# Kernel optimization log

Measured on AMD Instinct MI355X. Metric: run time of the kernel, lower is better.

The kernel has to match this reference:

```python
import jax, jax.numpy as jnp
import numpy as np

SEQ_LEN, PRED_LEN, PATCH_LEN, STRIDE, NUM_LAYERS = 512, 96, 16, 4, 2
NUM_QUBITS = 4
NUM_PATCHES = (SEQ_LEN - PATCH_LEN) // STRIDE + 1  # 125


def setup_inputs() -> dict:
    key = jax.random.key(0)
    k1, k2, k3, k4 = jax.random.split(key, 4)
    x = jax.random.normal(k1, (64, SEQ_LEN, 64), dtype=jnp.float32)
    weights = jax.random.uniform(k2, (NUM_LAYERS, NUM_QUBITS, 3), dtype=jnp.float32) * (2 * np.pi)
    head_w = jax.random.normal(k3, (PRED_LEN, NUM_PATCHES * NUM_QUBITS), dtype=jnp.float32) * 0.04
    head_b = jax.random.normal(k4, (PRED_LEN,), dtype=jnp.float32) * 0.01
    return {"x": x, "weights": weights, "head_w": head_w, "head_b": head_b}


def _apply_rot(state, phi, theta, omega, wire):
    # Rot = RZ(omega) RY(theta) RZ(phi); PennyLane wire 0 is MSB -> tensor axis wire+1
    c = jnp.cos(0.5 * theta)
    s = jnp.sin(0.5 * theta)
    e = lambda a: jnp.exp(1j * a)
    half, diff = 0.5 * (phi + omega), 0.5 * (phi - omega)
    U = jnp.stack([jnp.stack([e(-half) * c, -e(diff) * s]),
                   jnp.stack([e(-diff) * s, e(half) * c])]).astype(jnp.complex64)  # [2,2]
    st = jnp.moveaxis(state, wire + 1, -1)
    st = st @ U.T  # new_j = sum_k U[j,k] old_k
    return jnp.moveaxis(st, -1, wire + 1)


def _cnot(state, c, t):
    # flip target axis where control bit == 1
    mshape = [1, 1, 1, 1, 1]
    mshape[c + 1] = 2
    mask = (jnp.arange(2) == 1).reshape(mshape)
    return jnp.where(mask, jnp.flip(state, axis=t + 1), state)


def _quantum_encoder(patches, weights):
    # patches: [N,16] real; AmplitudeEmbedding(normalize=True)
    psi = patches / jnp.linalg.norm(patches, axis=-1, keepdims=True)
    state = psi.astype(jnp.complex64).reshape(-1, 2, 2, 2, 2)  # [N,2,2,2,2], wire0=MSB
    for l in range(NUM_LAYERS):
        for q in range(NUM_QUBITS):
            state = _apply_rot(state, weights[l, q, 0], weights[l, q, 1], weights[l, q, 2], q)
        r = (l % (NUM_QUBITS - 1)) + 1  # default StronglyEntanglingLayers ranges
        for i in range(NUM_QUBITS):
            state = _cnot(state, i, (i + r) % NUM_QUBITS)
    probs = jnp.abs(state.reshape(-1, 16)) ** 2  # [N,16]
    # <Z_q> = sum_k p_k * (1 - 2*bit_q(k)), wire0 = MSB of 4-bit index
    bits = (np.arange(16)[:, None] >> (NUM_QUBITS - 1 - np.arange(NUM_QUBITS))[None, :]) & 1
    signs = jnp.asarray(1.0 - 2.0 * bits, dtype=jnp.float32)  # [16,4]
    return probs @ signs  # [N,4]


def reference(x, weights, head_w, head_b):
    B, L, M = x.shape
    xs = jnp.transpose(x, (0, 2, 1)).reshape(B * M, L)
    idx = np.arange(NUM_PATCHES)[:, None] * STRIDE + np.arange(PATCH_LEN)[None, :]
    xp = xs[:, idx].reshape(-1, PATCH_LEN) + 1e-6  # [B*M*NP, 16]
    enc = _quantum_encoder(xp, weights)  # [B*M*NP, 4]
    enc = enc.reshape(B * M, NUM_PATCHES * NUM_QUBITS)
    out = enc @ head_w.T + head_b  # [B*M, pred_len]
    return jnp.transpose(out.reshape(B, M, PRED_LEN), (0, 2, 1))
```

## Files before the change

### kernel.cpp

```cpp
#include <hip/hip_runtime.h>
#include <cmath>

#define BATCH 64
#define SEQLEN 512
#define NFEAT 64
#define NPATCH 125
#define PREDLEN 96
#define NCOLS 500

#define MG 8
#define XROW 528
#define ELD 520

typedef __attribute__((ext_vector_type(8))) short short8;
typedef __attribute__((ext_vector_type(4))) short short4v;
typedef __attribute__((ext_vector_type(4))) float f32x4;

__device__ __forceinline__ unsigned short f2bf(float f) {
    unsigned int u = __float_as_uint(f);
    u += 0x7FFFu + ((u >> 16) & 1u);
    return (unsigned short)(u >> 16);
}
__device__ __forceinline__ float bf2f(unsigned short h) {
    return __uint_as_float(((unsigned int)h) << 16);
}
__device__ __forceinline__ unsigned int cvtpk(float a, float b) {
    unsigned int r;
    asm volatile("v_cvt_pk_bf16_f32 %0, %1, %2" : "=v"(r) : "v"(a), "v"(b));
    return r;
}

__global__ __launch_bounds__(512) void qml_one(
    const float* __restrict__ x,
    const float* __restrict__ w,
    const float* __restrict__ hw,
    const float* __restrict__ hb,
    float* __restrict__ out)
{
    __shared__ float G[32 * 16];
    __shared__ unsigned short xh[MG][XROW];
    __shared__ unsigned short xl[MG][XROW];
    __shared__ unsigned short enc[MG][ELD];

    const int tid  = threadIdx.x;
    const int lane = tid & 63;
    const int lr   = lane & 15;
    const int kg   = lane >> 4;
    const int wv   = tid >> 6;

    const int idx = blockIdx.x;
    const int b   = ((idx >> 6) << 3) | (idx & 7);
    const int m0  = ((idx >> 3) & 7) * MG;

    if (wv == 0) {
        float my[8];
        {
            const int  g      = lane & 7;
            const float phi   = w[g * 3 + 0];
            const float theta = w[g * 3 + 1];
            const float omega = w[g * 3 + 2];
            const float c  = cosf(0.5f * theta), s  = sinf(0.5f * theta);
            const float hf = 0.5f * (phi + omega), df = 0.5f * (phi - omega);
            const float ch = cosf(hf), sh = sinf(hf);
            const float cd = cosf(df), sd = sinf(df);
            my[0] =  ch * c;  my[1] = -sh * c;
            my[2] = -cd * s;  my[3] = -sd * s;
            my[4] =  cd * s;  my[5] = -sd * s;
            my[6] =  ch * c;  my[7] =  sh * c;
        }
        float re[16], im[16];
        #pragma unroll
        for (int k = 0; k < 16; ++k) { re[k] = (k == (lane & 15)) ? 1.f : 0.f; im[k] = 0.f; }
        #pragma unroll
        for (int l = 0; l < 2; ++l) {
            #pragma unroll
            for (int qq = 0; qq < 4; ++qq) {
                const int g = l * 4 + qq;
                const float u00r = __shfl(my[0], g), u00i = __shfl(my[1], g);
                const float u01r = __shfl(my[2], g), u01i = __shfl(my[3], g);
                const float u10r = __shfl(my[4], g), u10i = __shfl(my[5], g);
                const float u11r = __shfl(my[6], g), u11i = __shfl(my[7], g);
                const int bit = 8 >> qq;
                #pragma unroll
                for (int k = 0; k < 16; ++k) {
                    if (k & bit) continue;
                    const int k1 = k | bit;
                    const float a0r = re[k],  a0i = im[k];
                    const float a1r = re[k1], a1i = im[k1];
                    re[k]  = u00r * a0r - u00i * a0i + u01r * a1r - u01i * a1i;
                    im[k]  = u00r * a0i + u00i * a0r + u01r * a1i + u01i * a1r;
                    re[k1] = u10r * a0r - u10i * a0i + u11r * a1r - u11i * a1i;
                    im[k1] = u10r * a0i + u10i * a0r + u11r * a1i + u11i * a1r;
                }
            }
            const int r = (l % 3) + 1;
            #pragma unroll
            for (int i = 0; i < 4; ++i) {
                const int cb = 8 >> i;
                const int tb = 8 >> ((i + r) & 3);
                #pragma unroll
                for (int k = 0; k < 16; ++k) {
                    if ((k & cb) && !(k & tb)) {
                        const int k1 = k | tb;
                        float t;
                        t = re[k]; re[k] = re[k1]; re[k1] = t;
                        t = im[k]; im[k] = im[k1]; im[k1] = t;
                    }
                }
            }
        }
        if (lane < 16) {
            #pragma unroll
            for (int k = 0; k < 16; ++k) {
                G[k * 16 + lane]        = re[k];
                G[(16 + k) * 16 + lane] = im[k];
            }
        }
    } else {
        const float* xb = x + (size_t)b * SEQLEN * NFEAT + m0;
        unsigned int* xh32[8]; unsigned int* xl32[8];
        #pragma unroll
        for (int c = 0; c < 8; ++c) {
            xh32[c] = reinterpret_cast<unsigned int*>(&xh[c][0]);
            xl32[c] = reinterpret_cast<unsigned int*>(&xl[c][0]);
        }
        for (int u = tid - 64; u < XROW / 2; u += 448) {
            const int t = 2 * u;
            float4 a0, a1, b0, b1;
            if (t < SEQLEN) {
                const float* base = xb + (size_t)t * NFEAT;
                a0 = *reinterpret_cast<const float4*>(base);
                a1 = *reinterpret_cast<const float4*>(base + 4);
                b0 = *reinterpret_cast<const float4*>(base + NFEAT);
                b1 = *reinterpret_cast<const float4*>(base + NFEAT + 4);
            } else {
                a0 = make_float4(0.f, 0.f, 0.f, 0.f);
                a1 = a0; b0 = a0; b1 = a0;
            }
            const float av[8] = {a0.x, a0.y, a0.z, a0.w, a1.x, a1.y, a1.z, a1.w};
            const float bv[8] = {b0.x, b0.y, b0.z, b0.w, b1.x, b1.y, b1.z, b1.w};
            #pragma unroll
            for (int c = 0; c < 8; ++c) {
                const float va = av[c] + 1e-6f;
                const float vb = bv[c] + 1e-6f;
                const unsigned int h = cvtpk(va, vb);
                xh32[c][u] = h;
                const float ra = va - __uint_as_float(h << 16);
                const float rb = vb - __uint_as_float(h & 0xFFFF0000u);
                xl32[c][u] = cvtpk(ra, rb);
            }
        }
    }
    __syncthreads();

    short8 ah0, al0, ah1, al1;
    {
        const int koff = (kg & 1) * 8;
        #pragma unroll
        for (int c = 0; c < 8; ++c) {
            const float g0 = G[lr * 16 + koff + c];
            const unsigned short h0 = f2bf(g0);
            ah0[c] = (short)h0;
            al0[c] = (short)f2bf(g0 - bf2f(h0));
            const float g1 = G[(16 + lr) * 16 + koff + c];
            const unsigned short h1 = f2bf(g1);
            ah1[c] = (short)h1;
            al1[c] = (short)f2bf(g1 - bf2f(h1));
        }
    }

    {
        const int m = wv;
        const unsigned short* xrow = (kg < 2) ? &xh[m][0] : &xl[m][0];
        #pragma unroll 1
        for (int nt = 0; nt < 8; ++nt) {
            const int p = nt * 16 + lr;

            const short4v* src = reinterpret_cast<const short4v*>(xrow + 4 * p + (kg & 1) * 8);
            const short4v s0 = src[0];
            const short4v s1 = src[1];
            short8 bfrag;
            #pragma unroll
            for (int c = 0; c < 4; ++c) { bfrag[c] = s0[c]; bfrag[c + 4] = s1[c]; }

            const f32x4 zz = {0.f, 0.f, 0.f, 0.f};
            f32x4 acc0 = __builtin_amdgcn_mfma_f32_16x16x32_bf16(al0, bfrag, zz, 0, 0, 0);
            acc0 = __builtin_amdgcn_mfma_f32_16x16x32_bf16(ah0, bfrag, acc0, 0, 0, 0);
            f32x4 acc1 = __builtin_amdgcn_mfma_f32_16x16x32_bf16(al1, bfrag, zz, 0, 0, 0);
            acc1 = __builtin_amdgcn_mfma_f32_16x16x32_bf16(ah1, bfrag, acc1, 0, 0, 0);

            const float p0 = acc0[0] * acc0[0] + acc1[0] * acc1[0];
            const float p1 = acc0[1] * acc0[1] + acc1[1] * acc1[1];
            const float p2 = acc0[2] * acc0[2] + acc1[2] * acc1[2];
            const float p3 = acc0[3] * acc0[3] + acc1[3] * acc1[3];
            const float psum = (p0 + p1) + (p2 + p3);
            float s0v = (kg & 2) ? psum : 0.f;
            float s1v = (kg & 1) ? psum : 0.f;
            float s2v = p2 + p3;
            float s3v = p1 + p3;
            float sav = psum;
            s0v += __shfl_xor(s0v, 16); s0v += __shfl_xor(s0v, 32);
            s1v += __shfl_xor(s1v, 16); s1v += __shfl_xor(s1v, 32);
            s2v += __shfl_xor(s2v, 16); s2v += __shfl_xor(s2v, 32);
            s3v += __shfl_xor(s3v, 16); s3v += __shfl_xor(s3v, 32);
            sav += __shfl_xor(sav, 16); sav += __shfl_xor(sav, 32);

            const float rinv = 1.f / sav;
            const float ssel = (kg == 0) ? s0v : (kg == 1) ? s1v : (kg == 2) ? s2v : s3v;
            const float zval = 1.f - 2.f * ssel * rinv;
            enc[m][4 * p + kg] = (p < NPATCH) ? f2bf(zval) : (unsigned short)0;
        }
    }
    __syncthreads();

    if (wv < 6) {
        const int o = wv * 16 + lr;
        const float* hwrow = hw + (size_t)o * NCOLS;
        const unsigned short* erow = &enc[lr & 7][0];

        f32x4 acc = {0.f, 0.f, 0.f, 0.f};
        #pragma unroll 2
        for (int kc = 0; kc < 15; ++kc) {
            const int k0 = kc * 32 + kg * 8;
            const short8 e  = *reinterpret_cast<const short8*>(erow + k0);
            const float4 w0 = *reinterpret_cast<const float4*>(hwrow + k0);
            const float4 w1 = *reinterpret_cast<const float4*>(hwrow + k0 + 4);
            union { unsigned int u[4]; short8 s; } wf;
            wf.u[0] = cvtpk(w0.x, w0.y);
            wf.u[1] = cvtpk(w0.z, w0.w);
            wf.u[2] = cvtpk(w1.x, w1.y);
            wf.u[3] = cvtpk(w1.z, w1.w);
            acc = __builtin_amdgcn_mfma_f32_16x16x32_bf16(e, wf.s, acc, 0, 0, 0);
        }
        {
            const int k0 = 480 + kg * 8;
            const short8 e = *reinterpret_cast<const short8*>(erow + k0);
            short8 wf;
            #pragma unroll
            for (int c = 0; c < 8; ++c) {
                const int k = k0 + c;
                wf[c] = (k < NCOLS) ? (short)f2bf(hwrow[k]) : (short)0;
            }
            acc = __builtin_amdgcn_mfma_f32_16x16x32_bf16(e, wf, acc, 0, 0, 0);
        }

        if (kg < 2) {
            const float bias = hb[o];
            #pragma unroll
            for (int j = 0; j < 4; ++j) {
                const int m = m0 + 4 * kg + j;
                out[((size_t)b * PREDLEN + o) * NFEAT + m] = acc[j] + bias;
            }
        }
    }
}

extern "C" void kernel_launch(void* const* d_in, const int* in_sizes, int n_in,
                              void* d_out, int out_size, void* d_ws, size_t ws_size,
                              hipStream_t stream) {
    const float* x  = (const float*)d_in[0];
    const float* w  = (const float*)d_in[1];
    const float* hw = (const float*)d_in[2];
    const float* hb = (const float*)d_in[3];
    float* out = (float*)d_out;

    (void)d_ws; (void)ws_size; (void)in_sizes; (void)n_in; (void)out_size;
    qml_one<<<dim3(BATCH * (NFEAT / MG)), dim3(512), 0, stream>>>(x, w, hw, hb, out);
}
```

Before: 26.87 us.

## Use 32x32x16 MFMA for quantum encoder with 3-term split-bf16 product

```diff
diff --git a/kernel.cpp b/kernel.cpp
--- a/kernel.cpp
+++ b/kernel.cpp
@@ -14,7 +14,9 @@
 
 typedef __attribute__((ext_vector_type(8))) short short8;
 typedef __attribute__((ext_vector_type(4))) short short4v;
+typedef __attribute__((ext_vector_type(4))) unsigned short ushort4v;
 typedef __attribute__((ext_vector_type(4))) float f32x4;
+typedef __attribute__((ext_vector_type(16))) float f32x16;
 
 __device__ __forceinline__ unsigned short f2bf(float f) {
     unsigned int u = __float_as_uint(f);
@@ -44,8 +46,6 @@
 
     const int tid  = threadIdx.x;
     const int lane = tid & 63;
-    const int lr   = lane & 15;
-    const int kg   = lane >> 4;
     const int wv   = tid >> 6;
 
     const int idx = blockIdx.x;
@@ -153,73 +153,94 @@
     }
     __syncthreads();
 
-    short8 ah0, al0, ah1, al1;
     {
-        const int koff = (kg & 1) * 8;
-        #pragma unroll
-        for (int c = 0; c < 8; ++c) {
-            const float g0 = G[lr * 16 + koff + c];
-            const unsigned short h0 = f2bf(g0);
-            ah0[c] = (short)h0;
-            al0[c] = (short)f2bf(g0 - bf2f(h0));
-            const float g1 = G[(16 + lr) * 16 + koff + c];
-            const unsigned short h1 = f2bf(g1);
-            ah1[c] = (short)h1;
-            al1[c] = (short)f2bf(g1 - bf2f(h1));
-        }
-    }
-
-    {
-        const int m = wv;
-        const unsigned short* xrow = (kg < 2) ? &xh[m][0] : &xl[m][0];
+        const int m  = wv;
+        const int pl = lane & 31;
+        const int hi = lane >> 5;
+        const int j0 = hi * 8;
+
+        short8 gah, gal;
+        {
+            const int r = lane & 31;
+            #pragma unroll
+            for (int c = 0; c < 8; ++c) {
+                const float g = G[r * 16 + j0 + c];
+                const unsigned short h = f2bf(g);
+                gah[c] = (short)h;
+                gal[c] = (short)f2bf(g - bf2f(h));
+            }
+        }
+
+        const unsigned short* xhr = &xh[m][0];
+        const unsigned short* xlr = &xl[m][0];
         #pragma unroll 1
-        for (int nt = 0; nt < 8; ++nt) {
-            const int p = nt * 16 + lr;
-
-            const short4v* src = reinterpret_cast<const short4v*>(xrow + 4 * p + (kg & 1) * 8);
-            const short4v s0 = src[0];
-            const short4v s1 = src[1];
-            short8 bfrag;
-            #pragma unroll
-            for (int c = 0; c < 4; ++c) { bfrag[c] = s0[c]; bfrag[c + 4] = s1[c]; }
-
-            const f32x4 zz = {0.f, 0.f, 0.f, 0.f};
-            f32x4 acc0 = __builtin_amdgcn_mfma_f32_16x16x32_bf16(al0, bfrag, zz, 0, 0, 0);
-            acc0 = __builtin_amdgcn_mfma_f32_16x16x32_bf16(ah0, bfrag, acc0, 0, 0, 0);
-            f32x4 acc1 = __builtin_amdgcn_mfma_f32_16x16x32_bf16(al1, bfrag, zz, 0, 0, 0);
-            acc1 = __builtin_amdgcn_mfma_f32_16x16x32_bf16(ah1, bfrag, acc1, 0, 0, 0);
-
-            const float p0 = acc0[0] * acc0[0] + acc1[0] * acc1[0];
-            const float p1 = acc0[1] * acc0[1] + acc1[1] * acc1[1];
-            const float p2 = acc0[2] * acc0[2] + acc1[2] * acc1[2];
-            const float p3 = acc0[3] * acc0[3] + acc1[3] * acc1[3];
-            const float psum = (p0 + p1) + (p2 + p3);
-            float s0v = (kg & 2) ? psum : 0.f;
-            float s1v = (kg & 1) ? psum : 0.f;
-            float s2v = p2 + p3;
-            float s3v = p1 + p3;
-            float sav = psum;
-            s0v += __shfl_xor(s0v, 16); s0v += __shfl_xor(s0v, 32);
-            s1v += __shfl_xor(s1v, 16); s1v += __shfl_xor(s1v, 32);
-            s2v += __shfl_xor(s2v, 16); s2v += __shfl_xor(s2v, 32);
-            s3v += __shfl_xor(s3v, 16); s3v += __shfl_xor(s3v, 32);
-            sav += __shfl_xor(sav, 16); sav += __shfl_xor(sav, 32);
-
-            const float rinv = 1.f / sav;
-            const float ssel = (kg == 0) ? s0v : (kg == 1) ? s1v : (kg == 2) ? s2v : s3v;
-            const float zval = 1.f - 2.f * ssel * rinv;
-            enc[m][4 * p + kg] = (p < NPATCH) ? f2bf(zval) : (unsigned short)0;
+        for (int nt = 0; nt < 4; ++nt) {
+            const int p = nt * 32 + pl;
+            const int base = 4 * p + j0;
+            const short4v h0 = *reinterpret_cast<const short4v*>(xhr + base);
+            const short4v h1 = *reinterpret_cast<const short4v*>(xhr + base + 4);
+            const short4v l0 = *reinterpret_cast<const short4v*>(xlr + base);
+            const short4v l1 = *reinterpret_cast<const short4v*>(xlr + base + 4);
+            short8 bh, bl;
+            #pragma unroll
+            for (int c = 0; c < 4; ++c) {
+                bh[c] = h0[c]; bh[c + 4] = h1[c];
+                bl[c] = l0[c]; bl[c + 4] = l1[c];
+            }
+
+            f32x16 D = {0.f, 0.f, 0.f, 0.f, 0.f, 0.f, 0.f, 0.f,
+                        0.f, 0.f, 0.f, 0.f, 0.f, 0.f, 0.f, 0.f};
+            D = __builtin_amdgcn_mfma_f32_32x32x16_bf16(gah, bh, D, 0, 0, 0);
+            D = __builtin_amdgcn_mfma_f32_32x32x16_bf16(gal, bh, D, 0, 0, 0);
+            D = __builtin_amdgcn_mfma_f32_32x32x16_bf16(gah, bl, D, 0, 0, 0);
+
+            float pi[8];
+            #pragma unroll
+            for (int i = 0; i < 8; ++i) pi[i] = D[i] * D[i] + D[i + 8] * D[i + 8];
+
+            const float sa_p = ((pi[0] + pi[1]) + (pi[2] + pi[3]))
+                             + ((pi[4] + pi[5]) + (pi[6] + pi[7]));
+            const float s0_p = (pi[4] + pi[5]) + (pi[6] + pi[7]);
+            const float s2_p = (pi[2] + pi[3]) + (pi[6] + pi[7]);
+            const float s3_p = (pi[1] + pi[3]) + (pi[5] + pi[7]);
+
+            const float o_sa = __shfl_xor(sa_p, 32);
+            const float o_s0 = __shfl_xor(s0_p, 32);
+            const float o_s2 = __shfl_xor(s2_p, 32);
+            const float o_s3 = __shfl_xor(s3_p, 32);
+
+            const float sa = sa_p + o_sa;
+            const float s0 = s0_p + o_s0;
+            const float s1 = hi ? sa_p : o_sa;
+            const float s2 = s2_p + o_s2;
+            const float s3 = s3_p + o_s3;
+
+            const float t  = -2.f / sa;
+            ushort4v zv;
+            if (p < NPATCH) {
+                zv[0] = f2bf(fmaf(t, s0, 1.f));
+                zv[1] = f2bf(fmaf(t, s1, 1.f));
+                zv[2] = f2bf(fmaf(t, s2, 1.f));
+                zv[3] = f2bf(fmaf(t, s3, 1.f));
+            } else {
+                zv[0] = 0; zv[1] = 0; zv[2] = 0; zv[3] = 0;
+            }
+            if (hi == 0) {
+                *reinterpret_cast<ushort4v*>(&enc[m][4 * p]) = zv;
+            }
         }
     }
     __syncthreads();
 
     if (wv < 6) {
-        const int o = wv * 16 + lr;
+        const int lr = lane & 15;
+        const int kg = lane >> 4;
+        const int o  = wv * 16 + lr;
         const float* hwrow = hw + (size_t)o * NCOLS;
         const unsigned short* erow = &enc[lr & 7][0];
 
         f32x4 acc = {0.f, 0.f, 0.f, 0.f};
-        #pragma unroll 2
+        #pragma unroll 4
         for (int kc = 0; kc < 15; ++kc) {
             const int k0 = kc * 32 + kg * 8;
             const short8 e  = *reinterpret_cast<const short8*>(erow + k0);
```

Result: faster. 23.61 us (-12.2%).
